# Kernel tuning notes

Hardware: AMD Instinct MI355X
Metric: run time of the kernel (lower is better)

## Reference

```python
import jax, jax.numpy as jnp
import numpy as np

N = 100000
E = 1600000
F_IN = 512
HID = 8
HEADS = 8
NUM_CLASSES = 40
NEG_SLOPE = 0.2


def setup_inputs() -> dict:
    key = jax.random.key(0)
    ks = jax.random.split(key, 12)
    x = jax.random.normal(ks[0], (N, F_IN), dtype=jnp.float32)
    edge_index = jax.random.randint(ks[1], (2, E), 0, N, dtype=jnp.int64)
    s1 = 1.0 / np.sqrt(F_IN)
    s2 = 1.0 / np.sqrt(HID * HEADS)
    W1 = jax.random.normal(ks[2], (F_IN, HEADS * HID), dtype=jnp.float32) * s1
    a_src1 = jax.random.normal(ks[3], (HEADS, HID), dtype=jnp.float32) * s1
    a_dst1 = jax.random.normal(ks[4], (HEADS, HID), dtype=jnp.float32) * s1
    b1 = jnp.zeros((HEADS * HID,), dtype=jnp.float32)
    W2 = jax.random.normal(ks[5], (HEADS * HID, NUM_CLASSES), dtype=jnp.float32) * s2
    a_src2 = jax.random.normal(ks[6], (1, NUM_CLASSES), dtype=jnp.float32) * s2
    a_dst2 = jax.random.normal(ks[7], (1, NUM_CLASSES), dtype=jnp.float32) * s2
    b2 = jnp.zeros((NUM_CLASSES,), dtype=jnp.float32)
    return {"x": x, "edge_index": edge_index, "W1": W1, "a_src1": a_src1,
            "a_dst1": a_dst1, "b1": b1, "W2": W2, "a_src2": a_src2,
            "a_dst2": a_dst2, "b2": b2}


def _gat_conv(x, src, dst, W, a_src, a_dst, b, heads, out_ch):
    # linear projection, per-head: [N, heads, out_ch]
    h = (x @ W).reshape(N, heads, out_ch)
    # per-node attention logits [N, heads]
    al_s = jnp.einsum('nhf,hf->nh', h, a_src)
    al_d = jnp.einsum('nhf,hf->nh', h, a_dst)
    # per-edge raw scores [E', heads]
    e = jax.nn.leaky_relu(al_s[src] + al_d[dst], NEG_SLOPE)
    # segment softmax over edges sharing a destination node
    m = jax.lax.stop_gradient(jax.ops.segment_max(e, dst, num_segments=N))
    m = jnp.where(jnp.isfinite(m), m, 0.0)
    e = jnp.exp(e - m[dst])
    denom = jax.ops.segment_sum(e, dst, num_segments=N)
    alpha = e / denom[dst]  # [E', heads]
    # scatter-weighted aggregation of gathered source features
    out = jax.ops.segment_sum(alpha[:, :, None] * h[src], dst, num_segments=N)
    return out.reshape(N, heads * out_ch) + b


def reference(x, edge_index, W1, a_src1, a_dst1, b1, W2, a_src2, a_dst2, b2):
    # PyG GATConv default: add self-loops
    loops = jnp.arange(N, dtype=edge_index.dtype)
    src = jnp.concatenate([edge_index[0], loops])
    dst = jnp.concatenate([edge_index[1], loops])
    h = _gat_conv(x, src, dst, W1, a_src1, a_dst1, b1, HEADS, HID)
    h = jax.nn.elu(h)
    # dropout(p=0.6) is identity in eval mode
    out = _gat_conv(h, src, dst, W2, a_src2, a_dst2, b2, 1, NUM_CLASSES)
    return jax.nn.log_softmax(out, axis=1)
```

## Files before the change

### kernel.cpp

```cpp
#include <hip/hip_runtime.h>
#include <hip/hip_bf16.h>
#include <cstdint>
#include <cstddef>

#define N_NODES 100000
#define N_EDGES 1600000
#define E_TOT   (N_EDGES + N_NODES)
#define F_IN    512
#define HEADS   8
#define HID     8
#define F_H     64
#define NC      40
#define NEG     0.2f

#define BSH    8
#define NB     391
#define CHUNKH 8192
#define NBH    ((E_TOT + CHUNKH - 1) / CHUNKH)
#define CHUNKF 4096
#define NBF    ((E_TOT + CHUNKF - 1) / CHUNKF)
#define CAP    7168
#define GEMM_G ((N_NODES + 63) / 64)
#define FG_T   (GEMM_G + NBF)
#define FG_R1  (NBF * 4)

typedef __attribute__((ext_vector_type(8))) __bf16 bf16x8;
typedef __attribute__((ext_vector_type(4))) float f32x4;
typedef __attribute__((ext_vector_type(8))) unsigned short u16x8;

__device__ __forceinline__ float bf2f(unsigned short u) {
  unsigned int w = ((unsigned int)u) << 16;
  return __builtin_bit_cast(float, w);
}
__device__ __forceinline__ unsigned short f2bf(float f) {
  __hip_bfloat16 b = __float2bfloat16(f);
  return __builtin_bit_cast(unsigned short, b);
}
__device__ __forceinline__ float lrexp(float v) {
  v = (v > 0.f) ? v : NEG * v;
  return __expf(v);
}

__device__ __forceinline__ bool detect_i64(const int* __restrict__ ei) {
  int lane = threadIdx.x & 63;
  int v = ei[2 * lane + 1];
  return __ballot(v != 0) == 0ull;
}

__device__ __forceinline__ int load_dst(const int* __restrict__ ei, bool f, int i) {
  if (i < N_EDGES) return f ? ei[2 * (N_EDGES + i)] : ei[N_EDGES + i];
  return i - N_EDGES;
}
__device__ __forceinline__ int load_src(const int* __restrict__ ei, bool f, int i) {
  if (i < N_EDGES) return f ? ei[2 * i] : ei[i];
  return i - N_EDGES;
}

__global__ __launch_bounds__(256) void k_hist_pack(
    const int* __restrict__ ei, const float* __restrict__ W1,
    uint4* __restrict__ w1f, int* __restrict__ bcnt) {
  __shared__ int h[NB];
  const int t = threadIdx.x;
  if (blockIdx.x < 16) {
    int tid = blockIdx.x * 256 + t;
    int lane = tid & 63;
    int tt = (tid >> 6) & 3;
    int s = tid >> 8;
    int k0 = s * 32 + ((lane >> 4) << 3);
    int col = tt * 16 + (lane & 15);
    u16x8 v;
#pragma unroll
    for (int i = 0; i < 8; ++i) v[i] = f2bf(W1[(size_t)(k0 + i) * F_H + col]);
    w1f[tid] = __builtin_bit_cast(uint4, v);
    return;
  }
  const int blk = blockIdx.x - 16;
  const bool f = detect_i64(ei);
  for (int i = t; i < NB; i += 256) h[i] = 0;
  __syncthreads();
  const int base = blk * CHUNKH;
#pragma unroll
  for (int j = 0; j < CHUNKH / 256; ++j) {
    int i = base + t + j * 256;
    if (i < E_TOT) atomicAdd(&h[load_dst(ei, f, i) >> BSH], 1);
  }
  __syncthreads();
  for (int i = t; i < NB; i += 256)
    if (h[i]) atomicAdd(&bcnt[i], h[i]);
}

__global__ __launch_bounds__(512) void k_bscan(const int* __restrict__ bcnt,
                                               int* __restrict__ bstart,
                                               int* __restrict__ bcur,
                                               int* __restrict__ rowstart) {
  __shared__ int sh[512];
  const int t = threadIdx.x;
  int v = (t < NB) ? bcnt[t] : 0;
  sh[t] = v;
  __syncthreads();
  for (int d = 1; d < 512; d <<= 1) {
    int u = (t >= d) ? sh[t - d] : 0;
    __syncthreads();
    sh[t] += u;
    __syncthreads();
  }
  if (t < NB) {
    int e = sh[t] - v;
    bstart[t] = e;
    bcur[t] = e;
  }
  if (t == 0) { bstart[NB] = E_TOT; rowstart[N_NODES] = E_TOT; }
}

__global__ __launch_bounds__(256) void k_fill_gemm(
    const int* __restrict__ ei, int* __restrict__ bcur,
    unsigned int* __restrict__ inter,
    const float* __restrict__ x, const uint4* __restrict__ w1f,
    const float* __restrict__ a_src, const float* __restrict__ a_dst,
    unsigned short* __restrict__ h1b, float* __restrict__ als,
    float* __restrict__ ald) {
  __shared__ unsigned int ent[CHUNKF];
  __shared__ int h[NB], ofs[NB], cur[NB], gpos[NB];
  const int b = (int)blockIdx.x;
  const int t = threadIdx.x;
  bool isFill;
  int idx;
  if (b < FG_R1) {
    if ((b & 3) == 3) { isFill = true;  idx = b >> 2; }
    else              { isFill = false; idx = b - (b >> 2); }
  } else {
    isFill = false; idx = b - NBF;
  }

  if (isFill) {
    const bool f = detect_i64(ei);
    const int base = idx * CHUNKF;
    for (int i = t; i < NB; i += 256) h[i] = 0;
    __syncthreads();
#pragma unroll
    for (int j = 0; j < CHUNKF / 256; ++j) {
      int i = base + t + j * 256;
      if (i < E_TOT) atomicAdd(&h[load_dst(ei, f, i) >> BSH], 1);
    }
    __syncthreads();
    if (t < 64) {
      int loc[7];
      int s = 0;
#pragma unroll
      for (int k = 0; k < 7; ++k) {
        int ix = t * 7 + k;
        int hv = (ix < NB) ? h[ix] : 0;
        loc[k] = s;
        s += hv;
      }
      int incl = s;
      for (int dd = 1; dd < 64; dd <<= 1) {
        int u = __shfl_up(incl, dd);
        if (t >= dd) incl += u;
      }
      int excl = incl - s;
#pragma unroll
      for (int k = 0; k < 7; ++k) {
        int ix = t * 7 + k;
        if (ix < NB) ofs[ix] = excl + loc[k];
      }
    }
    __syncthreads();
    for (int i = t; i < NB; i += 256) {
      cur[i] = ofs[i];
      gpos[i] = h[i] ? atomicAdd(&bcur[i], h[i]) : 0;
    }
    __syncthreads();
#pragma unroll
    for (int j = 0; j < CHUNKF / 256; ++j) {
      int i = base + t + j * 256;
      if (i < E_TOT) {
        int s = load_src(ei, f, i);
        int d = load_dst(ei, f, i);
        int p = atomicAdd(&cur[d >> BSH], 1);
        ent[p] = ((unsigned int)(d & 255) << 24) | (unsigned int)s;
      }
    }
    __syncthreads();
    const int wv = t >> 6, ln = t & 63;
    for (int bb = wv; bb < NB; bb += 4) {
      int c = h[bb];
      if (!c) continue;
      int g = gpos[bb], o = ofs[bb];
      for (int i = ln; i < c; i += 64) inter[g + i] = ent[o + i];
    }
    return;
  }

  const int lane = t & 63;
  const int wv = t >> 6;
  const int rb = idx * 64 + wv * 16;
  int arow = rb + (lane & 15);
  if (arow >= N_NODES) arow = N_NODES - 1;
  const float* aptr = x + (size_t)arow * F_IN + ((lane >> 4) << 3);

  f32x4 acc[4];
#pragma unroll
  for (int i = 0; i < 4; ++i) acc[i] = (f32x4){0.f, 0.f, 0.f, 0.f};

#pragma unroll 4
  for (int s = 0; s < 16; ++s) {
    float4 a0 = *reinterpret_cast<const float4*>(aptr + s * 32);
    float4 a1 = *reinterpret_cast<const float4*>(aptr + s * 32 + 4);
    uint4 b0 = w1f[(s * 4 + 0) * 64 + lane];
    uint4 b1 = w1f[(s * 4 + 1) * 64 + lane];
    uint4 b2 = w1f[(s * 4 + 2) * 64 + lane];
    uint4 b3 = w1f[(s * 4 + 3) * 64 + lane];
    bf16x8 af;
    af[0] = (__bf16)a0.x; af[1] = (__bf16)a0.y;
    af[2] = (__bf16)a0.z; af[3] = (__bf16)a0.w;
    af[4] = (__bf16)a1.x; af[5] = (__bf16)a1.y;
    af[6] = (__bf16)a1.z; af[7] = (__bf16)a1.w;
    acc[0] = __builtin_amdgcn_mfma_f32_16x16x32_bf16(af, __builtin_bit_cast(bf16x8, b0), acc[0], 0, 0, 0);
    acc[1] = __builtin_amdgcn_mfma_f32_16x16x32_bf16(af, __builtin_bit_cast(bf16x8, b1), acc[1], 0, 0, 0);
    acc[2] = __builtin_amdgcn_mfma_f32_16x16x32_bf16(af, __builtin_bit_cast(bf16x8, b2), acc[2], 0, 0, 0);
    acc[3] = __builtin_amdgcn_mfma_f32_16x16x32_bf16(af, __builtin_bit_cast(bf16x8, b3), acc[3], 0, 0, 0);
  }

  const int r0 = rb + ((lane >> 4) << 2);
  const int c = lane & 15;
#pragma unroll
  for (int tt = 0; tt < 4; ++tt) {
#pragma unroll
    for (int i = 0; i < 4; ++i) {
      int r = r0 + i;
      if (r < N_NODES) h1b[(size_t)r * F_H + tt * 16 + c] = f2bf(acc[tt][i]);
    }
  }

  float asw[4], adw[4];
#pragma unroll
  for (int tt = 0; tt < 4; ++tt) {
    asw[tt] = a_src[tt * 16 + c];
    adw[tt] = a_dst[tt * 16 + c];
  }
  float sp[4][4], dp[4][4];
#pragma unroll
  for (int tt = 0; tt < 4; ++tt)
#pragma unroll
    for (int i = 0; i < 4; ++i) {
      sp[tt][i] = acc[tt][i] * asw[tt];
      dp[tt][i] = acc[tt][i] * adw[tt];
    }
#pragma unroll
  for (int dd = 1; dd < 8; dd <<= 1)
#pragma unroll
    for (int tt = 0; tt < 4; ++tt)
#pragma unroll
      for (int i = 0; i < 4; ++i) {
        sp[tt][i] += __shfl_xor(sp[tt][i], dd);
        dp[tt][i] += __shfl_xor(dp[tt][i], dd);
      }
  if ((c & 7) == 0) {
    const int hb = c >> 3;
#pragma unroll
    for (int i = 0; i < 4; ++i) {
      int r = r0 + i;
      if (r < N_NODES) {
#pragma unroll
        for (int tt = 0; tt < 4; ++tt) {
          als[(size_t)r * HEADS + tt * 2 + hb] = sp[tt][i];
          ald[(size_t)r * HEADS + tt * 2 + hb] = dp[tt][i];
        }
      }
    }
  }
}

__global__ __launch_bounds__(256) void k_cfill(const unsigned int* __restrict__ inter,
                                               const int* __restrict__ bstart,
                                               int* __restrict__ rowstart,
                                               int* __restrict__ csrc) {
  __shared__ unsigned int out_l[CAP];
  __shared__ int cnt[256], sc[256], cur2[256];
  const int t = threadIdx.x;
  const int b = blockIdx.x;
  const int segStart = bstart[b];
  const int L = bstart[b + 1] - segStart;
  cnt[t] = 0;
  __syncthreads();
  for (int i = t; i < L; i += 256) atomicAdd(&cnt[inter[segStart + i] >> 24], 1);
  __syncthreads();
  sc[t] = cnt[t];
  __syncthreads();
  for (int d = 1; d < 256; d <<= 1) {
    int v = (t >= d) ? sc[t - d] : 0;
    __syncthreads();
    sc[t] += v;
    __syncthreads();
  }
  const int excl = sc[t] - cnt[t];
  cur2[t] = excl;
  const int node = (b << BSH) + t;
  if (node < N_NODES) rowstart[node] = segStart + excl;
  __syncthreads();
  if (L <= CAP) {
    for (int i = t; i < L; i += 256) {
      unsigned int e = inter[segStart + i];
      int p = atomicAdd(&cur2[e >> 24], 1);
      out_l[p] = e & 0xFFFFFFu;
    }
    __syncthreads();
    for (int i = t; i < L; i += 256) csrc[segStart + i] = (int)out_l[i];
  } else {
    for (int i = t; i < L; i += 256) {
      unsigned int e = inter[segStart + i];
      int p = atomicAdd(&cur2[e >> 24], 1);
      csrc[segStart + p] = (int)(e & 0xFFFFFFu);
    }
  }
}

__global__ __launch_bounds__(256) void k_agg1n(
    const int* __restrict__ rowstart, const int* __restrict__ csrc,
    const unsigned short* __restrict__ h1b, const float* __restrict__ als,
    const float* __restrict__ ald, const float* __restrict__ b1,
    unsigned short* __restrict__ hactb) {
  const int w = (int)((blockIdx.x * 256 + threadIdx.x) >> 6);
  const int lane = threadIdx.x & 63;
  const int grp = lane >> 3;
  const int l = lane & 7;
  const int n = w * 8 + grp;
  const bool live = (n < N_NODES);
  const int e0 = live ? rowstart[n] : 0;
  const int e1 = live ? rowstart[n + 1] : 0;
  const float aldv = live ? ald[(size_t)n * HEADS + l] : 0.f;

  float den = 0.f;
  float acc[8];
#pragma unroll
  for (int k = 0; k < 8; ++k) acc[k] = 0.f;

  int e = e0;
  for (; e + 4 <= e1; e += 4) {
    int4 sv = *reinterpret_cast<const int4*>(&csrc[e]);
    float a0 = als[(size_t)sv.x * HEADS + l];
    float a1 = als[(size_t)sv.y * HEADS + l];
    float a2 = als[(size_t)sv.z * HEADS + l];
    float a3 = als[(size_t)sv.w * HEADS + l];
    uint4 u0 = *reinterpret_cast<const uint4*>(&h1b[(size_t)sv.x * F_H + l * 8]);
    uint4 u1 = *reinterpret_cast<const uint4*>(&h1b[(size_t)sv.y * F_H + l * 8]);
    uint4 u2 = *reinterpret_cast<const uint4*>(&h1b[(size_t)sv.z * F_H + l * 8]);
    uint4 u3 = *reinterpret_cast<const uint4*>(&h1b[(size_t)sv.w * F_H + l * 8]);
    float p0 = lrexp(a0 + aldv), p1 = lrexp(a1 + aldv);
    float p2 = lrexp(a2 + aldv), p3 = lrexp(a3 + aldv);
    den += (p0 + p1) + (p2 + p3);
    const unsigned int* q0 = &u0.x;
    const unsigned int* q1 = &u1.x;
    const unsigned int* q2 = &u2.x;
    const unsigned int* q3 = &u3.x;
#pragma unroll
    for (int k = 0; k < 4; ++k) {
      acc[2 * k]     += p0 * bf2f((unsigned short)q0[k]) + p1 * bf2f((unsigned short)q1[k])
                      + p2 * bf2f((unsigned short)q2[k]) + p3 * bf2f((unsigned short)q3[k]);
      acc[2 * k + 1] += p0 * bf2f((unsigned short)(q0[k] >> 16)) + p1 * bf2f((unsigned short)(q1[k] >> 16))
                      + p2 * bf2f((unsigned short)(q2[k] >> 16)) + p3 * bf2f((unsigned short)(q3[k] >> 16));
    }
  }
  for (; e < e1; ++e) {
    int s = csrc[e];
    float a = als[(size_t)s * HEADS + l];
    uint4 u = *reinterpret_cast<const uint4*>(&h1b[(size_t)s * F_H + l * 8]);
    float p = lrexp(a + aldv);
    den += p;
    const unsigned int* q = &u.x;
#pragma unroll
    for (int k = 0; k < 4; ++k) {
      acc[2 * k]     += p * bf2f((unsigned short)q[k]);
      acc[2 * k + 1] += p * bf2f((unsigned short)(q[k] >> 16));
    }
  }

  if (live) {
    float inv = 1.f / den;
    uint4 outw;
    unsigned int* ow = &outw.x;
#pragma unroll
    for (int k = 0; k < 4; ++k) {
      float ox = acc[2 * k] * inv + b1[l * 8 + 2 * k];
      float oy = acc[2 * k + 1] * inv + b1[l * 8 + 2 * k + 1];
      ox = (ox > 0.f) ? ox : expm1f(ox);
      oy = (oy > 0.f) ? oy : expm1f(oy);
      ow[k] = ((unsigned int)f2bf(oy) << 16) | (unsigned int)f2bf(ox);
    }
    *reinterpret_cast<uint4*>(&hactb[(size_t)n * F_H + l * 8]) = outw;
  }
}

__global__ __launch_bounds__(256) void k_l2proj(
    const unsigned short* __restrict__ hactb, const float* __restrict__ W2,
    const float* __restrict__ a_src2, const float* __restrict__ a_dst2,
    unsigned short* __restrict__ h2b, float* __restrict__ als2,
    float* __restrict__ ald2) {
  __shared__ float hs[64 * 68];
  __shared__ float w2s[F_H * NC];
  const int t = threadIdx.x;
  const int nb = blockIdx.x * 64;
  {
    int r0 = t >> 3, c8 = t & 7;
#pragma unroll
    for (int i = 0; i < 2; ++i) {
      int r = r0 + i * 32;
      int gr = nb + r;
      u16x8 v = (u16x8)(0);
      if (gr < N_NODES)
        v = *reinterpret_cast<const u16x8*>(&hactb[(size_t)gr * F_H + c8 * 8]);
#pragma unroll
      for (int k = 0; k < 8; ++k) hs[r * 68 + c8 * 8 + k] = bf2f(v[k]);
    }
  }
  for (int i = t; i < F_H * NC; i += 256) w2s[i] = W2[i];
  __syncthreads();

  const int node = t >> 2, cg = t & 3;
  float acc[10];
#pragma unroll
  for (int c = 0; c < 10; ++c) acc[c] = 0.f;
  for (int k = 0; k < F_H; ++k) {
    float xv = hs[node * 68 + k];
#pragma unroll
    for (int c = 0; c < 10; ++c) acc[c] += xv * w2s[k * NC + cg * 10 + c];
  }
  const int gn = nb + node;
  float ps = 0.f, pd = 0.f;
#pragma unroll
  for (int c = 0; c < 10; ++c) {
    ps += acc[c] * a_src2[cg * 10 + c];
    pd += acc[c] * a_dst2[cg * 10 + c];
  }
  ps += __shfl_xor(ps, 1); ps += __shfl_xor(ps, 2);
  pd += __shfl_xor(pd, 1); pd += __shfl_xor(pd, 2);
  if (gn < N_NODES) {
#pragma unroll
    for (int c = 0; c < 10; ++c) h2b[(size_t)gn * NC + cg * 10 + c] = f2bf(acc[c]);
    if (cg == 0) { als2[gn] = ps; ald2[gn] = pd; }
  }
}

__global__ __launch_bounds__(256) void k_agg2n(
    const int* __restrict__ rowstart, const int* __restrict__ csrc,
    const unsigned short* __restrict__ h2b, const float* __restrict__ als2,
    const float* __restrict__ ald2, const float* __restrict__ b2,
    float* __restrict__ out) {
  const int w = (int)((blockIdx.x * 256 + threadIdx.x) >> 6);
  const int lane = threadIdx.x & 63;
  const int grp = lane >> 3;
  const int l = lane & 7;
  const int n = w * 8 + grp;
  const bool live = (n < N_NODES);
  const int e0 = live ? rowstart[n] : 0;
  const int e1 = live ? rowstart[n + 1] : 0;
  const float aldv = live ? ald2[n] : 0.f;
  const bool act = (l < 5);
  const int fo = act ? l * 8 : 0;

  float den = 0.f;
  float acc[8];
#pragma unroll
  for (int k = 0; k < 8; ++k) acc[k] = 0.f;

  int e = e0;
  for (; e + 4 <= e1; e += 4) {
    int4 sv = *reinterpret_cast<const int4*>(&csrc[e]);
    float a0 = als2[sv.x], a1 = als2[sv.y], a2 = als2[sv.z], a3 = als2[sv.w];
    uint4 u0 = *reinterpret_cast<const uint4*>(&h2b[(size_t)sv.x * NC + fo]);
    uint4 u1 = *reinterpret_cast<const uint4*>(&h2b[(size_t)sv.y * NC + fo]);
    uint4 u2 = *reinterpret_cast<const uint4*>(&h2b[(size_t)sv.z * NC + fo]);
    uint4 u3 = *reinterpret_cast<const uint4*>(&h2b[(size_t)sv.w * NC + fo]);
    float p0 = lrexp(a0 + aldv), p1 = lrexp(a1 + aldv);
    float p2 = lrexp(a2 + aldv), p3 = lrexp(a3 + aldv);
    den += (p0 + p1) + (p2 + p3);
    const unsigned int* q0 = &u0.x;
    const unsigned int* q1 = &u1.x;
    const unsigned int* q2 = &u2.x;
    const unsigned int* q3 = &u3.x;
#pragma unroll
    for (int k = 0; k < 4; ++k) {
      acc[2 * k]     += p0 * bf2f((unsigned short)q0[k]) + p1 * bf2f((unsigned short)q1[k])
                      + p2 * bf2f((unsigned short)q2[k]) + p3 * bf2f((unsigned short)q3[k]);
      acc[2 * k + 1] += p0 * bf2f((unsigned short)(q0[k] >> 16)) + p1 * bf2f((unsigned short)(q1[k] >> 16))
                      + p2 * bf2f((unsigned short)(q2[k] >> 16)) + p3 * bf2f((unsigned short)(q3[k] >> 16));
    }
  }
  for (; e < e1; ++e) {
    int s = csrc[e];
    float a = als2[s];
    uint4 u = *reinterpret_cast<const uint4*>(&h2b[(size_t)s * NC + fo]);
    float p = lrexp(a + aldv);
    den += p;
    const unsigned int* q = &u.x;
#pragma unroll
    for (int k = 0; k < 4; ++k) {
      acc[2 * k]     += p * bf2f((unsigned short)q[k]);
      acc[2 * k + 1] += p * bf2f((unsigned short)(q[k] >> 16));
    }
  }

  float o[8];
  float inv = 1.f / den;
  float mx = -1e30f;
#pragma unroll
  for (int k = 0; k < 8; ++k) {
    o[k] = act ? (acc[k] * inv + b2[fo + k]) : -1e30f;
    mx = fmaxf(mx, o[k]);
  }
  mx = fmaxf(mx, __shfl_xor(mx, 1));
  mx = fmaxf(mx, __shfl_xor(mx, 2));
  mx = fmaxf(mx, __shfl_xor(mx, 4));
  float se = 0.f;
#pragma unroll
  for (int k = 0; k < 8; ++k) se += act ? __expf(o[k] - mx) : 0.f;
  se += __shfl_xor(se, 1);
  se += __shfl_xor(se, 2);
  se += __shfl_xor(se, 4);
  if (live && act) {
    float ls = __logf(se);
    float4 r0, r1;
    r0.x = o[0] - mx - ls; r0.y = o[1] - mx - ls;
    r0.z = o[2] - mx - ls; r0.w = o[3] - mx - ls;
    r1.x = o[4] - mx - ls; r1.y = o[5] - mx - ls;
    r1.z = o[6] - mx - ls; r1.w = o[7] - mx - ls;
    *reinterpret_cast<float4*>(&out[(size_t)n * NC + l * 8]) = r0;
    *reinterpret_cast<float4*>(&out[(size_t)n * NC + l * 8 + 4]) = r1;
  }
}

extern "C" void kernel_launch(void* const* d_in, const int* in_sizes, int n_in,
                              void* d_out, int out_size, void* d_ws, size_t ws_size,
                              hipStream_t stream) {
  const float* x      = (const float*)d_in[0];
  const int*   ei     = (const int*)d_in[1];
  const float* W1     = (const float*)d_in[2];
  const float* a_src1 = (const float*)d_in[3];
  const float* a_dst1 = (const float*)d_in[4];
  const float* b1     = (const float*)d_in[5];
  const float* W2     = (const float*)d_in[6];
  const float* a_src2 = (const float*)d_in[7];
  const float* a_dst2 = (const float*)d_in[8];
  const float* b2     = (const float*)d_in[9];
  float* out = (float*)d_out;

  char* ws = (char*)d_ws;
  size_t o = 0;
  auto carve = [&](size_t bytes) -> char* {
    char* p = ws + o;
    o = (o + bytes + 255) & ~(size_t)255;
    return p;
  };
  int*   bcnt     = (int*)carve((size_t)NB * 4);
  int*   bstart   = (int*)carve((size_t)(NB + 1) * 4);
  int*   bcur     = (int*)carve((size_t)NB * 4);
  int*   rowstart = (int*)carve((size_t)(N_NODES + 1) * 4);
  unsigned int* inter = (unsigned int*)carve((size_t)E_TOT * 4);
  int*   csrc     = (int*)carve((size_t)(E_TOT + 8) * 4);
  uint4* w1f      = (uint4*)carve((size_t)4096 * 16);
  unsigned short* h1b   = (unsigned short*)carve((size_t)N_NODES * F_H * 2);
  float* als1     = (float*)carve((size_t)N_NODES * HEADS * 4);
  float* ald1     = (float*)carve((size_t)N_NODES * HEADS * 4);
  unsigned short* hactb = (unsigned short*)carve((size_t)N_NODES * F_H * 2);
  unsigned short* h2b   = (unsigned short*)carve((size_t)(N_NODES * NC + 8) * 2);
  float* als2     = (float*)carve((size_t)N_NODES * 4);
  float* ald2     = (float*)carve((size_t)N_NODES * 4);
  (void)ws_size; (void)n_in; (void)in_sizes; (void)out_size;

  hipMemsetAsync(bcnt, 0, (size_t)NB * 4, stream);
  k_hist_pack<<<16 + NBH, 256, 0, stream>>>(ei, W1, w1f, bcnt);
  k_bscan<<<1, 512, 0, stream>>>(bcnt, bstart, bcur, rowstart);
  k_fill_gemm<<<FG_T, 256, 0, stream>>>(ei, bcur, inter, x, w1f, a_src1, a_dst1,
                                        h1b, als1, ald1);
  k_cfill<<<NB, 256, 0, stream>>>(inter, bstart, rowstart, csrc);

  const int aggGrid = (N_NODES + 31) / 32;
  k_agg1n<<<aggGrid, 256, 0, stream>>>(rowstart, csrc, h1b, als1, ald1, b1, hactb);
  k_l2proj<<<(N_NODES + 63) / 64, 256, 0, stream>>>(hactb, W2, a_src2, a_dst2, h2b, als2, ald2);
  k_agg2n<<<aggGrid, 256, 0, stream>>>(rowstart, csrc, h2b, als2, ald2, b2, out);
}
```

Baseline: 246.4 us.

## Split fused fill/GEMM kernel and stage x tiles through LDS

Splits the combined bucket-fill and layer-1 projection kernel into two separate kernels. The fill chunk size is doubled, so fewer fill blocks each do more work. The GEMM now stages 64x64 tiles of x through shared memory with coalesced float4 loads, replacing the strided per-lane direct reads. This gives up the overlap between the fill and GEMM work that the interleaved fused launch provided, and adds one extra launch plus a barrier per K-chunk.

```diff
diff --git a/kernel.cpp b/kernel.cpp
--- a/kernel.cpp
+++ b/kernel.cpp
@@ -17,12 +17,10 @@
 #define NB     391
 #define CHUNKH 8192
 #define NBH    ((E_TOT + CHUNKH - 1) / CHUNKH)
-#define CHUNKF 4096
+#define CHUNKF 8192
 #define NBF    ((E_TOT + CHUNKF - 1) / CHUNKF)
 #define CAP    7168
 #define GEMM_G ((N_NODES + 63) / 64)
-#define FG_T   (GEMM_G + NBF)
-#define FG_R1  (NBF * 4)
 
 typedef __attribute__((ext_vector_type(8))) __bf16 bf16x8;
 typedef __attribute__((ext_vector_type(4))) float f32x4;
@@ -112,117 +110,124 @@
   if (t == 0) { bstart[NB] = E_TOT; rowstart[N_NODES] = E_TOT; }
 }
 
-__global__ __launch_bounds__(256) void k_fill_gemm(
-    const int* __restrict__ ei, int* __restrict__ bcur,
-    unsigned int* __restrict__ inter,
+__global__ __launch_bounds__(256) void k_bfill(const int* __restrict__ ei,
+                                               int* __restrict__ bcur,
+                                               unsigned int* __restrict__ inter) {
+  __shared__ unsigned int ent[CHUNKF];
+  __shared__ int h[NB], ofs[NB], cur[NB], gpos[NB];
+  const int t = threadIdx.x;
+  const int base = blockIdx.x * CHUNKF;
+  const bool f = detect_i64(ei);
+  for (int i = t; i < NB; i += 256) h[i] = 0;
+  __syncthreads();
+#pragma unroll
+  for (int j = 0; j < CHUNKF / 256; ++j) {
+    int i = base + t + j * 256;
+    if (i < E_TOT) atomicAdd(&h[load_dst(ei, f, i) >> BSH], 1);
+  }
+  __syncthreads();
+  if (t < 64) {
+    int loc[7];
+    int s = 0;
+#pragma unroll
+    for (int k = 0; k < 7; ++k) {
+      int ix = t * 7 + k;
+      int hv = (ix < NB) ? h[ix] : 0;
+      loc[k] = s;
+      s += hv;
+    }
+    int incl = s;
+    for (int dd = 1; dd < 64; dd <<= 1) {
+      int u = __shfl_up(incl, dd);
+      if (t >= dd) incl += u;
+    }
+    int excl = incl - s;
+#pragma unroll
+    for (int k = 0; k < 7; ++k) {
+      int ix = t * 7 + k;
+      if (ix < NB) ofs[ix] = excl + loc[k];
+    }
+  }
+  __syncthreads();
+  for (int i = t; i < NB; i += 256) {
+    cur[i] = ofs[i];
+    gpos[i] = h[i] ? atomicAdd(&bcur[i], h[i]) : 0;
+  }
+  __syncthreads();
+#pragma unroll
+  for (int j = 0; j < CHUNKF / 256; ++j) {
+    int i = base + t + j * 256;
+    if (i < E_TOT) {
+      int s = load_src(ei, f, i);
+      int d = load_dst(ei, f, i);
+      int p = atomicAdd(&cur[d >> BSH], 1);
+      ent[p] = ((unsigned int)(d & 255) << 24) | (unsigned int)s;
+    }
+  }
+  __syncthreads();
+  const int wv = t >> 6, ln = t & 63;
+  for (int b = wv; b < NB; b += 4) {
+    int c = h[b];
+    if (!c) continue;
+    int g = gpos[b], o = ofs[b];
+    for (int i = ln; i < c; i += 64) inter[g + i] = ent[o + i];
+  }
+}
+
+__global__ __launch_bounds__(256) void k_gemm1s(
     const float* __restrict__ x, const uint4* __restrict__ w1f,
     const float* __restrict__ a_src, const float* __restrict__ a_dst,
     unsigned short* __restrict__ h1b, float* __restrict__ als,
     float* __restrict__ ald) {
-  __shared__ unsigned int ent[CHUNKF];
-  __shared__ int h[NB], ofs[NB], cur[NB], gpos[NB];
-  const int b = (int)blockIdx.x;
+  constexpr int PITCH = 68;
+  __shared__ float xs[64 * PITCH];
   const int t = threadIdx.x;
-  bool isFill;
-  int idx;
-  if (b < FG_R1) {
-    if ((b & 3) == 3) { isFill = true;  idx = b >> 2; }
-    else              { isFill = false; idx = b - (b >> 2); }
-  } else {
-    isFill = false; idx = b - NBF;
-  }
-
-  if (isFill) {
-    const bool f = detect_i64(ei);
-    const int base = idx * CHUNKF;
-    for (int i = t; i < NB; i += 256) h[i] = 0;
-    __syncthreads();
-#pragma unroll
-    for (int j = 0; j < CHUNKF / 256; ++j) {
-      int i = base + t + j * 256;
-      if (i < E_TOT) atomicAdd(&h[load_dst(ei, f, i) >> BSH], 1);
-    }
-    __syncthreads();
-    if (t < 64) {
-      int loc[7];
-      int s = 0;
-#pragma unroll
-      for (int k = 0; k < 7; ++k) {
-        int ix = t * 7 + k;
-        int hv = (ix < NB) ? h[ix] : 0;
-        loc[k] = s;
-        s += hv;
-      }
-      int incl = s;
-      for (int dd = 1; dd < 64; dd <<= 1) {
-        int u = __shfl_up(incl, dd);
-        if (t >= dd) incl += u;
-      }
-      int excl = incl - s;
-#pragma unroll
-      for (int k = 0; k < 7; ++k) {
-        int ix = t * 7 + k;
-        if (ix < NB) ofs[ix] = excl + loc[k];
-      }
-    }
-    __syncthreads();
-    for (int i = t; i < NB; i += 256) {
-      cur[i] = ofs[i];
-      gpos[i] = h[i] ? atomicAdd(&bcur[i], h[i]) : 0;
-    }
-    __syncthreads();
-#pragma unroll
-    for (int j = 0; j < CHUNKF / 256; ++j) {
-      int i = base + t + j * 256;
-      if (i < E_TOT) {
-        int s = load_src(ei, f, i);
-        int d = load_dst(ei, f, i);
-        int p = atomicAdd(&cur[d >> BSH], 1);
-        ent[p] = ((unsigned int)(d & 255) << 24) | (unsigned int)s;
-      }
-    }
-    __syncthreads();
-    const int wv = t >> 6, ln = t & 63;
-    for (int bb = wv; bb < NB; bb += 4) {
-      int c = h[bb];
-      if (!c) continue;
-      int g = gpos[bb], o = ofs[bb];
-      for (int i = ln; i < c; i += 64) inter[g + i] = ent[o + i];
-    }
-    return;
-  }
-
   const int lane = t & 63;
   const int wv = t >> 6;
-  const int rb = idx * 64 + wv * 16;
-  int arow = rb + (lane & 15);
-  if (arow >= N_NODES) arow = N_NODES - 1;
-  const float* aptr = x + (size_t)arow * F_IN + ((lane >> 4) << 3);
+  const int rb = blockIdx.x * 64;
+  const int srow = t >> 4;
+  const int scol = t & 15;
+  const int myrow = wv * 16 + (lane & 15);
+  const int koff = (lane >> 4) << 3;
 
   f32x4 acc[4];
 #pragma unroll
   for (int i = 0; i < 4; ++i) acc[i] = (f32x4){0.f, 0.f, 0.f, 0.f};
 
-#pragma unroll 4
-  for (int s = 0; s < 16; ++s) {
-    float4 a0 = *reinterpret_cast<const float4*>(aptr + s * 32);
-    float4 a1 = *reinterpret_cast<const float4*>(aptr + s * 32 + 4);
-    uint4 b0 = w1f[(s * 4 + 0) * 64 + lane];
-    uint4 b1 = w1f[(s * 4 + 1) * 64 + lane];
-    uint4 b2 = w1f[(s * 4 + 2) * 64 + lane];
-    uint4 b3 = w1f[(s * 4 + 3) * 64 + lane];
-    bf16x8 af;
-    af[0] = (__bf16)a0.x; af[1] = (__bf16)a0.y;
-    af[2] = (__bf16)a0.z; af[3] = (__bf16)a0.w;
-    af[4] = (__bf16)a1.x; af[5] = (__bf16)a1.y;
-    af[6] = (__bf16)a1.z; af[7] = (__bf16)a1.w;
-    acc[0] = __builtin_amdgcn_mfma_f32_16x16x32_bf16(af, __builtin_bit_cast(bf16x8, b0), acc[0], 0, 0, 0);
-    acc[1] = __builtin_amdgcn_mfma_f32_16x16x32_bf16(af, __builtin_bit_cast(bf16x8, b1), acc[1], 0, 0, 0);
-    acc[2] = __builtin_amdgcn_mfma_f32_16x16x32_bf16(af, __builtin_bit_cast(bf16x8, b2), acc[2], 0, 0, 0);
-    acc[3] = __builtin_amdgcn_mfma_f32_16x16x32_bf16(af, __builtin_bit_cast(bf16x8, b3), acc[3], 0, 0, 0);
-  }
-
-  const int r0 = rb + ((lane >> 4) << 2);
+  for (int kc = 0; kc < F_IN; kc += 64) {
+    __syncthreads();
+#pragma unroll
+    for (int j = 0; j < 4; ++j) {
+      int r = srow + j * 16;
+      int gr = rb + r;
+      float4 v = make_float4(0.f, 0.f, 0.f, 0.f);
+      if (gr < N_NODES)
+        v = *reinterpret_cast<const float4*>(&x[(size_t)gr * F_IN + kc + scol * 4]);
+      *reinterpret_cast<float4*>(&xs[r * PITCH + scol * 4]) = v;
+    }
+    __syncthreads();
+#pragma unroll
+    for (int s2 = 0; s2 < 2; ++s2) {
+      const int sg = (kc >> 5) + s2;
+      float4 a0 = *reinterpret_cast<const float4*>(&xs[myrow * PITCH + s2 * 32 + koff]);
+      float4 a1 = *reinterpret_cast<const float4*>(&xs[myrow * PITCH + s2 * 32 + koff + 4]);
+      uint4 b0 = w1f[(sg * 4 + 0) * 64 + lane];
+      uint4 b1 = w1f[(sg * 4 + 1) * 64 + lane];
+      uint4 b2 = w1f[(sg * 4 + 2) * 64 + lane];
+      uint4 b3 = w1f[(sg * 4 + 3) * 64 + lane];
+      bf16x8 af;
+      af[0] = (__bf16)a0.x; af[1] = (__bf16)a0.y;
+      af[2] = (__bf16)a0.z; af[3] = (__bf16)a0.w;
+      af[4] = (__bf16)a1.x; af[5] = (__bf16)a1.y;
+      af[6] = (__bf16)a1.z; af[7] = (__bf16)a1.w;
+      acc[0] = __builtin_amdgcn_mfma_f32_16x16x32_bf16(af, __builtin_bit_cast(bf16x8, b0), acc[0], 0, 0, 0);
+      acc[1] = __builtin_amdgcn_mfma_f32_16x16x32_bf16(af, __builtin_bit_cast(bf16x8, b1), acc[1], 0, 0, 0);
+      acc[2] = __builtin_amdgcn_mfma_f32_16x16x32_bf16(af, __builtin_bit_cast(bf16x8, b2), acc[2], 0, 0, 0);
+      acc[3] = __builtin_amdgcn_mfma_f32_16x16x32_bf16(af, __builtin_bit_cast(bf16x8, b3), acc[3], 0, 0, 0);
+    }
+  }
+
+  const int r0 = rb + wv * 16 + ((lane >> 4) << 2);
   const int c = lane & 15;
 #pragma unroll
   for (int tt = 0; tt < 4; ++tt) {
@@ -571,8 +576,8 @@
   hipMemsetAsync(bcnt, 0, (size_t)NB * 4, stream);
   k_hist_pack<<<16 + NBH, 256, 0, stream>>>(ei, W1, w1f, bcnt);
   k_bscan<<<1, 512, 0, stream>>>(bcnt, bstart, bcur, rowstart);
-  k_fill_gemm<<<FG_T, 256, 0, stream>>>(ei, bcur, inter, x, w1f, a_src1, a_dst1,
-                                        h1b, als1, ald1);
+  k_bfill<<<NBF, 256, 0, stream>>>(ei, bcur, inter);
+  k_gemm1s<<<GEMM_G, 256, 0, stream>>>(x, w1f, a_src1, a_dst1, h1b, als1, ald1);
   k_cfill<<<NB, 256, 0, stream>>>(inter, bstart, rowstart, csrc);
 
   const int aggGrid = (N_NODES + 31) / 32;
```

Result: slower. 271.3 us (+10.1%).
